# Performance work log

Measured on AMD Instinct MI355X. Metric: run time of the kernel, lower is better.

The kernel has to match this reference:

```python
import jax, jax.numpy as jnp
import numpy as np

B, C, H, W = 4, 256, 48, 48
NH = 4                 # num_heads
HD = C // NH           # head_dim = 64
KD = HD // 2           # key_dim = 32 (attn_ratio=0.5)
QKV_C = C + 2 * KD * NH  # 512
FF = 2 * C             # 512
EPS = 1e-3             # ultralytics BatchNorm2d eps


def _bn(x, g, b, m, v):
    # eval-mode BatchNorm2d over channel dim 1 of NCHW
    s = g / jnp.sqrt(v + EPS)
    return x * s[:, None, None] + (b - m * s)[:, None, None]


def _conv1x1(x, w):
    # w: [out_c, in_c]
    return jnp.einsum('bchw,oc->bohw', x, w)


def _dwconv3x3(x, w):
    # depthwise 3x3, padding 1; w: [C, 1, 3, 3]
    return jax.lax.conv_general_dilated(
        x, w, (1, 1), [(1, 1), (1, 1)],
        dimension_numbers=('NCHW', 'OIHW', 'NCHW'),
        feature_group_count=C)


def setup_inputs() -> dict:
    key = jax.random.key(0)
    ks = jax.random.split(key, 32)
    d = {}
    d['x'] = jax.random.normal(ks[0], (B, C, H, W), dtype=jnp.float32)

    def bn_params(i, ch):
        g = 0.5 + jax.random.uniform(ks[i], (ch,), dtype=jnp.float32)
        b = 0.1 * jax.random.normal(ks[i + 1], (ch,), dtype=jnp.float32)
        m = 0.1 * jax.random.normal(ks[i + 2], (ch,), dtype=jnp.float32)
        v = 0.5 + jax.random.uniform(ks[i + 3], (ch,), dtype=jnp.float32)
        return g, b, m, v

    d['qkv_w'] = 0.05 * jax.random.normal(ks[1], (QKV_C, C), dtype=jnp.float32)
    d['qkv_g'], d['qkv_b'], d['qkv_m'], d['qkv_v'] = bn_params(2, QKV_C)
    d['pe_w'] = 0.1 * jax.random.normal(ks[6], (C, 1, 3, 3), dtype=jnp.float32)
    d['pe_g'], d['pe_b'], d['pe_m'], d['pe_v'] = bn_params(7, C)
    d['proj_w'] = 0.05 * jax.random.normal(ks[11], (C, C), dtype=jnp.float32)
    d['proj_g'], d['proj_b'], d['proj_m'], d['proj_v'] = bn_params(12, C)
    d['f1_w'] = 0.05 * jax.random.normal(ks[16], (FF, C), dtype=jnp.float32)
    d['f1_g'], d['f1_b'], d['f1_m'], d['f1_v'] = bn_params(17, FF)
    d['f2_w'] = 0.05 * jax.random.normal(ks[21], (C, FF), dtype=jnp.float32)
    d['f2_g'], d['f2_b'], d['f2_m'], d['f2_v'] = bn_params(22, C)
    return d


def reference(x, qkv_w, qkv_g, qkv_b, qkv_m, qkv_v,
              pe_w, pe_g, pe_b, pe_m, pe_v,
              proj_w, proj_g, proj_b, proj_m, proj_v,
              f1_w, f1_g, f1_b, f1_m, f1_v,
              f2_w, f2_g, f2_b, f2_m, f2_v):
    b, c, h, w = x.shape
    n = h * w
    # --- Attention ---
    qkv = _bn(_conv1x1(x, qkv_w), qkv_g, qkv_b, qkv_m, qkv_v)
    qkv = qkv.reshape(b, NH, 2 * KD + HD, n)
    q = qkv[:, :, :KD]            # [b, nh, kd, n]
    k = qkv[:, :, KD:2 * KD]      # [b, nh, kd, n]
    v = qkv[:, :, 2 * KD:]        # [b, nh, hd, n]
    attn = jnp.einsum('bhkn,bhkm->bhnm', q, k) * (KD ** -0.5)
    attn = jax.nn.softmax(attn, axis=-1)
    o = jnp.einsum('bhdm,bhnm->bhdn', v, attn).reshape(b, c, h, w)
    pe = _bn(_dwconv3x3(v.reshape(b, c, h, w), pe_w), pe_g, pe_b, pe_m, pe_v)
    attn_out = _bn(_conv1x1(o + pe, proj_w), proj_g, proj_b, proj_m, proj_v)
    x = x + attn_out  # shortcut
    # --- FFN ---
    f = _conv1x1(x, f1_w)
    f = _bn(f, f1_g, f1_b, f1_m, f1_v)
    f = f * jax.nn.sigmoid(f)  # SiLU
    f = _bn(_conv1x1(f, f2_w), f2_g, f2_b, f2_m, f2_v)
    return x + f  # shortcut
```

## Files before the change

kernel.cpp:

```cpp
#include <hip/hip_runtime.h>
#include <math.h>

#define Bb   4
#define Cc   256
#define Hh   48
#define Ww   48
#define NNp  2304
#define Rr   9216
#define NHd  4
#define QKVC 512
#define EPSf 1e-3f

typedef unsigned int   u32;
typedef unsigned short u16;
typedef __attribute__((ext_vector_type(8))) __bf16 bf16x8;
typedef __attribute__((ext_vector_type(4))) float  f32x4;

#if __has_builtin(__builtin_amdgcn_exp2f)
#define EXP2F(x) __builtin_amdgcn_exp2f(x)
#else
#define EXP2F(x) __expf((x) * 0.6931471805599453f)
#endif

__device__ __forceinline__ u16 f2bf(float f) {
    u32 u = __float_as_uint(f);
    u = (u + 0x7fffu + ((u >> 16) & 1u)) >> 16;
    return (u16)u;
}
__device__ __forceinline__ float bf2f(u16 h) {
    return __uint_as_float((u32)h << 16);
}
__device__ __forceinline__ u32 pk2bf(float a, float b) {
    union { __bf16 h; u16 u; } ua, ub;
    ua.h = (__bf16)a; ub.h = (__bf16)b;
    return (u32)ua.u | ((u32)ub.u << 16);
}
__device__ __forceinline__ void gload16(const void* gsrc, void* ldst) {
    __builtin_amdgcn_global_load_lds(
        (const __attribute__((address_space(1))) u32*)gsrc,
        (__attribute__((address_space(3))) u32*)ldst, 16, 0, 0);
}

__global__ __launch_bounds__(64)
void prep_all(const float* __restrict__ W0, const float* __restrict__ g0, const float* __restrict__ b0, const float* __restrict__ m0, const float* __restrict__ v0, u16* __restrict__ Wb0, float* __restrict__ bi0,
              const float* __restrict__ W1, const float* __restrict__ g1, const float* __restrict__ b1, const float* __restrict__ m1, const float* __restrict__ v1, u16* __restrict__ Wb1, float* __restrict__ bi1,
              const float* __restrict__ W2, const float* __restrict__ g2, const float* __restrict__ b2, const float* __restrict__ m2, const float* __restrict__ v2, u16* __restrict__ Wb2, float* __restrict__ bi2,
              const float* __restrict__ W3, const float* __restrict__ g3, const float* __restrict__ b3, const float* __restrict__ m3, const float* __restrict__ v3, u16* __restrict__ Wb3, float* __restrict__ bi3)
{
    const int bid = blockIdx.x;
    const float *W, *gp, *bp, *mp, *vp;
    u16* Wb; float* bias;
    int K = 256, oc;
    float c = 1.f;
    if (bid < 512) {
        oc = bid; W = W0; gp = g0; bp = b0; mp = m0; vp = v0; Wb = Wb0; bias = bi0;
        if ((oc & 127) < 32) c = 0.17677669529663687f * 1.4426950408889634f;
    } else if (bid < 768) {
        oc = bid - 512; W = W1; gp = g1; bp = b1; mp = m1; vp = v1; Wb = Wb1; bias = bi1;
    } else if (bid < 1280) {
        oc = bid - 768; W = W2; gp = g2; bp = b2; mp = m2; vp = v2; Wb = Wb2; bias = bi2;
    } else {
        oc = bid - 1280; W = W3; gp = g3; bp = b3; mp = m3; vp = v3; Wb = Wb3; bias = bi3;
        K = 512;
    }
    const int lane = threadIdx.x;
    const float s = gp[oc] * rsqrtf(vp[oc] + EPSf);
    if (lane == 0) bias[oc] = (bp[oc] - mp[oc] * s) * c;
    const float sc = s * c;
    for (int k0 = lane * 4; k0 < K; k0 += 256) {
        const float4 w = *(const float4*)(W + (size_t)oc * K + k0);
        u32 lo = (u32)f2bf(w.x * sc) | ((u32)f2bf(w.y * sc) << 16);
        u32 hi = (u32)f2bf(w.z * sc) | ((u32)f2bf(w.w * sc) << 16);
        *(uint2*)(Wb + (size_t)oc * K + k0) = make_uint2(lo, hi);
    }
}

__global__ __launch_bounds__(256)
void cvt_x(const float* __restrict__ x, u16* __restrict__ Xt)
{
    const int b = blockIdx.z, c0 = blockIdx.y * 64, n0 = blockIdx.x * 64;
    __shared__ float tile[64][65];
    const int tid = threadIdx.x;
    {
        const int n = tid & 63, cl = tid >> 6;
        #pragma unroll
        for (int cc = 0; cc < 16; ++cc) {
            const int c = cc * 4 + cl;
            tile[c][n] = x[((size_t)b * Cc + c0 + c) * NNp + n0 + n];
        }
    }
    __syncthreads();
    {
        const int n = tid >> 2, q = tid & 3;
        #pragma unroll
        for (int j = 0; j < 2; ++j) {
            const int ch = q * 2 + j, c = ch * 8;
            u32 w[4];
            #pragma unroll
            for (int e = 0; e < 4; ++e)
                w[e] = (u32)f2bf(tile[c + 2*e][n]) | ((u32)f2bf(tile[c + 2*e + 1][n]) << 16);
            *(uint4*)(Xt + ((size_t)b * NNp + n0 + n) * Cc + c0 + c)
                = make_uint4(w[0], w[1], w[2], w[3]);
        }
    }
}

template<int BN_, int FN_, int MODE>
__global__ __launch_bounds__(256)
void gemm_mfma(const u16* __restrict__ A, const u16* __restrict__ Bx,
               const float* __restrict__ bias, const float* __restrict__ resid,
               float* __restrict__ Yf, u16* __restrict__ Yt, int M, int K)
{
    constexpr int WN = FN_ * 16;
    const int r0 = blockIdx.x * BN_;
    const int m0 = blockIdx.y * 128;
    const int tid = threadIdx.x;
    const int lane = tid & 63, wid = tid >> 6;
    const int g = lane >> 4, i16 = lane & 15;
    const int wr = wid >> 1, wc = wid & 1;

    __shared__ __align__(16) u16 Al[2][4][128][8];
    __shared__ __align__(16) u16 Bl[2][4][BN_][8];

    f32x4 acc[4][FN_];
    #pragma unroll
    for (int i = 0; i < 4; ++i)
        #pragma unroll
        for (int j = 0; j < FN_; ++j) acc[i][j] = (f32x4){0.f, 0.f, 0.f, 0.f};

    #pragma unroll
    for (int ii = 0; ii < 2; ++ii) {
        const int ci = ii * 256 + tid;
        gload16(A + (size_t)(m0 + (ci & 127)) * K + (ci >> 7) * 8,
                (u16*)&Al[0][0][0][0] + (size_t)ci * 8);
    }
    if (BN_ == 128) {
        #pragma unroll
        for (int ii = 0; ii < 2; ++ii) {
            const int ci = ii * 256 + tid;
            gload16(Bx + (size_t)(r0 + (ci & 127)) * K + (ci >> 7) * 8,
                    (u16*)&Bl[0][0][0][0] + (size_t)ci * 8);
        }
    } else {
        gload16(Bx + (size_t)(r0 + (tid & 63)) * K + (tid >> 6) * 8,
                (u16*)&Bl[0][0][0][0] + (size_t)tid * 8);
    }
    __syncthreads();

    int buf = 0;
    for (int k0 = 0; k0 < K; k0 += 32) {
        if (k0 + 32 < K) {
            const int kn = k0 + 32;
            #pragma unroll
            for (int ii = 0; ii < 2; ++ii) {
                const int ci = ii * 256 + tid;
                gload16(A + (size_t)(m0 + (ci & 127)) * K + kn + (ci >> 7) * 8,
                        (u16*)&Al[buf ^ 1][0][0][0] + (size_t)ci * 8);
            }
            if (BN_ == 128) {
                #pragma unroll
                for (int ii = 0; ii < 2; ++ii) {
                    const int ci = ii * 256 + tid;
                    gload16(Bx + (size_t)(r0 + (ci & 127)) * K + kn + (ci >> 7) * 8,
                            (u16*)&Bl[buf ^ 1][0][0][0] + (size_t)ci * 8);
                }
            } else {
                gload16(Bx + (size_t)(r0 + (tid & 63)) * K + kn + (tid >> 6) * 8,
                        (u16*)&Bl[buf ^ 1][0][0][0] + (size_t)tid * 8);
            }
        }
        bf16x8 af[4], bf[FN_];
        #pragma unroll
        for (int ao = 0; ao < 4; ++ao)
            af[ao] = *(const bf16x8*)&Al[buf][g][wr * 64 + ao * 16 + i16][0];
        #pragma unroll
        for (int bo = 0; bo < FN_; ++bo)
            bf[bo] = *(const bf16x8*)&Bl[buf][g][wc * WN + bo * 16 + i16][0];
        __builtin_amdgcn_s_setprio(1);
        #pragma unroll
        for (int ao = 0; ao < 4; ++ao)
            #pragma unroll
            for (int bo = 0; bo < FN_; ++bo)
                acc[ao][bo] = __builtin_amdgcn_mfma_f32_16x16x32_bf16(
                    af[ao], bf[bo], acc[ao][bo], 0, 0, 0);
        __builtin_amdgcn_s_setprio(0);
        __syncthreads();
        buf ^= 1;
    }

    const int b  = r0 / NNp;
    const int nb = r0 - b * NNp;
    #pragma unroll
    for (int ao = 0; ao < 4; ++ao) {
        const int oc0 = m0 + wr * 64 + ao * 16 + g * 4;
        const float4 t4 = *(const float4*)(bias + oc0);
        #pragma unroll
        for (int bo = 0; bo < FN_; ++bo) {
            const int nloc = wc * WN + bo * 16 + i16;
            float y[4];
            y[0] = acc[ao][bo][0] + t4.x;  y[1] = acc[ao][bo][1] + t4.y;
            y[2] = acc[ao][bo][2] + t4.z;  y[3] = acc[ao][bo][3] + t4.w;
            if (MODE == 1 || MODE == 3) {
                const int n = nb + nloc;
                const size_t base = ((size_t)b * M + oc0) * NNp + n;
                #pragma unroll
                for (int r = 0; r < 4; ++r) {
                    y[r] += resid[base + (size_t)r * NNp];
                    Yf[base + (size_t)r * NNp] = y[r];
                }
            }
            if (MODE == 2) {
                #pragma unroll
                for (int r = 0; r < 4; ++r) y[r] = y[r] / (1.f + __expf(-y[r]));
            }
            if (MODE != 3) {
                const size_t rG = (size_t)(r0 + nloc);
                u32 lo = (u32)f2bf(y[0]) | ((u32)f2bf(y[1]) << 16);
                u32 hi = (u32)f2bf(y[2]) | ((u32)f2bf(y[3]) << 16);
                *(uint2*)(Yt + rG * M + oc0) = make_uint2(lo, hi);
            }
        }
    }
}

__global__ __launch_bounds__(256)
void repack_v(const u16* __restrict__ Yt, u16* __restrict__ Vb)
{
    const int m0 = blockIdx.x * 64;
    const int h = blockIdx.y, b = blockIdx.z;
    const int bh = b * NHd + h;
    __shared__ u16 vt[64][72];
    const int tid = threadIdx.x;
    #pragma unroll
    for (int ii = 0; ii < 2; ++ii) {
        const int mm = ii * 32 + (tid >> 3);
        const int ch = tid & 7;
        *(uint4*)&vt[mm][ch * 8] =
            *(const uint4*)(Yt + ((size_t)b * NNp + m0 + mm) * QKVC + h * 128 + 64 + ch * 8);
    }
    __syncthreads();
    const int d = tid >> 2, mq = tid & 3;
    #pragma unroll
    for (int j = 0; j < 2; ++j) {
        const int mc = mq * 2 + j;
        u32 w[4];
        #pragma unroll
        for (int e = 0; e < 4; ++e)
            w[e] = (u32)vt[mc * 8 + 2*e][d] | ((u32)vt[mc * 8 + 2*e + 1][d] << 16);
        *(uint4*)(Vb + ((size_t)bh * 64 + d) * NNp + m0 + mc * 8)
            = make_uint4(w[0], w[1], w[2], w[3]);
    }
}

__global__ __launch_bounds__(256)
void attn_mfma(const u16* __restrict__ Yt, const u16* __restrict__ Vb,
               u16* __restrict__ Ot)
{
    __shared__ __align__(16) u16 Klds[2][4][128][8];
    __shared__ __align__(16) u16 Vlds[2][64][16][8];
    __shared__ __align__(16) u32 Plds[4][2][16][36];

    const int tid  = threadIdx.x;
    const int wid  = tid >> 6;
    const int lane = tid & 63;
    const int g    = lane >> 4;
    const int i16  = lane & 15;
    const int ksl  = wid >> 1;
    const int qh   = wid & 1;

    const int h = blockIdx.y, b = blockIdx.z;
    const int bh = b * NHd + h;
    const size_t bG = (size_t)b * NNp;
    const u16* Vg = Vb + (size_t)bh * 64 * NNp;

    const int nq0 = blockIdx.x * 64 + qh * 32 + i16;
    bf16x8 qfrag[2];
    qfrag[0] = *(const bf16x8*)(Yt + (bG + nq0) * QKVC + h * 128 + g * 8);
    qfrag[1] = *(const bf16x8*)(Yt + (bG + nq0 + 16) * QKVC + h * 128 + g * 8);

    bf16x8 ones;
    { uint4 ov = make_uint4(0x3f803f80u, 0x3f803f80u, 0x3f803f80u, 0x3f803f80u);
      ones = *(bf16x8*)&ov; }

    const f32x4 zero = {0.f, 0.f, 0.f, 0.f};
    f32x4 oacc[2][4];
    f32x4 lacc[2];
    #pragma unroll
    for (int f = 0; f < 2; ++f) {
        lacc[f] = zero;
        #pragma unroll
        for (int d = 0; d < 4; ++d) oacc[f][d] = zero;
    }
    float m_run[2] = {-1e30f, -1e30f};

    #pragma unroll
    for (int ii = 0; ii < 2; ++ii) {
        const int ci = ii * 256 + tid;
        gload16(Yt + (bG + (ci & 127)) * QKVC + h * 128 + 32 + (ci >> 7) * 8,
                (u16*)&Klds[0][0][0][0] + (size_t)ci * 8);
    }
    #pragma unroll
    for (int ii = 0; ii < 4; ++ii) {
        const int idx = ii * 256 + tid;
        const int d = idx >> 4, cp = idx & 15;
        gload16(Vg + (size_t)d * NNp + (cp ^ (d & 7)) * 8,
                (u16*)&Vlds[0][0][0][0] + (size_t)idx * 8);
    }
    __syncthreads();

    int cur = 0;
    for (int t = 0; t < 18; ++t) {
        if (t < 17) {
            const int m0 = (t + 1) * 128;
            #pragma unroll
            for (int ii = 0; ii < 2; ++ii) {
                const int ci = ii * 256 + tid;
                gload16(Yt + (bG + m0 + (ci & 127)) * QKVC + h * 128 + 32 + (ci >> 7) * 8,
                        (u16*)&Klds[cur ^ 1][0][0][0] + (size_t)ci * 8);
            }
            #pragma unroll
            for (int ii = 0; ii < 4; ++ii) {
                const int idx = ii * 256 + tid;
                const int d = idx >> 4, cp = idx & 15;
                gload16(Vg + (size_t)d * NNp + m0 + (cp ^ (d & 7)) * 8,
                        (u16*)&Vlds[cur ^ 1][0][0][0] + (size_t)idx * 8);
            }
        }

        bf16x8 kf[4];
        #pragma unroll
        for (int j = 0; j < 4; ++j)
            kf[j] = *(const bf16x8*)&Klds[cur][g][ksl * 64 + 16 * j + i16][0];

        f32x4 sac[2][4];
        __builtin_amdgcn_s_setprio(1);
        #pragma unroll
        for (int f = 0; f < 2; ++f)
            #pragma unroll
            for (int j = 0; j < 4; ++j)
                sac[f][j] = __builtin_amdgcn_mfma_f32_16x16x32_bf16(
                    kf[j], qfrag[f], zero, 0, 0, 0);
        __builtin_amdgcn_s_setprio(0);

        #pragma unroll
        for (int f = 0; f < 2; ++f) {
            float pm = sac[f][0][0];
            #pragma unroll
            for (int j = 0; j < 4; ++j)
                #pragma unroll
                for (int r = 0; r < 4; ++r) pm = fmaxf(pm, sac[f][j][r]);
            pm = fmaxf(pm, __shfl_xor(pm, 16));
            pm = fmaxf(pm, __shfl_xor(pm, 32));

            if (!__all(pm <= m_run[f] + 8.f)) {
                const float mn = fmaxf(m_run[f], pm);
                const float fc = EXP2F(m_run[f] - mn);
                m_run[f] = mn;
                lacc[f][0] *= fc; lacc[f][1] *= fc;
                lacc[f][2] *= fc; lacc[f][3] *= fc;
                #pragma unroll
                for (int d = 0; d < 4; ++d) {
                    oacc[f][d][0] *= fc; oacc[f][d][1] *= fc;
                    oacc[f][d][2] *= fc; oacc[f][d][3] *= fc;
                }
            }

            u32* prow = &Plds[wid][f][i16][0];
            #pragma unroll
            for (int j = 0; j < 4; ++j) {
                const float p0 = EXP2F(sac[f][j][0] - m_run[f]);
                const float p1 = EXP2F(sac[f][j][1] - m_run[f]);
                const float p2 = EXP2F(sac[f][j][2] - m_run[f]);
                const float p3 = EXP2F(sac[f][j][3] - m_run[f]);
                *(uint2*)&prow[8 * j + 2 * g] = make_uint2(pk2bf(p0, p1), pk2bf(p2, p3));
            }
        }

        __builtin_amdgcn_s_setprio(1);
        #pragma unroll
        for (int s = 0; s < 2; ++s) {
            const bf16x8 pf0 = *(const bf16x8*)&Plds[wid][0][i16][16 * s + 4 * g];
            const bf16x8 pf1 = *(const bf16x8*)&Plds[wid][1][i16][16 * s + 4 * g];
            lacc[0] = __builtin_amdgcn_mfma_f32_16x16x32_bf16(ones, pf0, lacc[0], 0, 0, 0);
            lacc[1] = __builtin_amdgcn_mfma_f32_16x16x32_bf16(ones, pf1, lacc[1], 0, 0, 0);
            const int cv = ksl * 8 + 4 * s + g;
            #pragma unroll
            for (int db = 0; db < 4; ++db) {
                const bf16x8 vf = *(const bf16x8*)&Vlds[cur][db * 16 + i16][cv ^ (i16 & 7)][0];
                oacc[0][db] = __builtin_amdgcn_mfma_f32_16x16x32_bf16(vf, pf0, oacc[0][db], 0, 0, 0);
                oacc[1][db] = __builtin_amdgcn_mfma_f32_16x16x32_bf16(vf, pf1, oacc[1][db], 0, 0, 0);
            }
        }
        __builtin_amdgcn_s_setprio(0);

        __syncthreads();
        cur ^= 1;
    }

    float* Ml = (float*)&Vlds[0][0][0][0];
    if (wid >= 2) {
        #pragma unroll
        for (int f = 0; f < 2; ++f) {
            float* dst = Ml + ((size_t)((qh * 2 + f) * 64 + lane)) * 20;
            dst[0] = m_run[f];
            dst[1] = lacc[f][0];
            #pragma unroll
            for (int db = 0; db < 4; ++db)
                #pragma unroll
                for (int e = 0; e < 4; ++e)
                    dst[2 + db * 4 + e] = oacc[f][db][e];
        }
    }
    __syncthreads();
    if (wid < 2) {
        #pragma unroll
        for (int f = 0; f < 2; ++f) {
            const float* src = Ml + ((size_t)((qh * 2 + f) * 64 + lane)) * 20;
            const float m2 = src[0], l2 = src[1];
            const float mn = fmaxf(m_run[f], m2);
            const float fa = EXP2F(m_run[f] - mn);
            const float fb = EXP2F(m2 - mn);
            const float linv = 1.f / (lacc[f][0] * fa + l2 * fb);
            u16* ob = Ot + (bG + nq0 + f * 16) * Cc + h * 64;
            #pragma unroll
            for (int db = 0; db < 4; ++db) {
                const float y0 = (oacc[f][db][0] * fa + src[2 + db * 4 + 0] * fb) * linv;
                const float y1 = (oacc[f][db][1] * fa + src[2 + db * 4 + 1] * fb) * linv;
                const float y2 = (oacc[f][db][2] * fa + src[2 + db * 4 + 2] * fb) * linv;
                const float y3 = (oacc[f][db][3] * fa + src[2 + db * 4 + 3] * fb) * linv;
                *(uint2*)(ob + db * 16 + g * 4) =
                    make_uint2(pk2bf(y0, y1), pk2bf(y2, y3));
            }
        }
    }
}

__global__ __launch_bounds__(256)
void pe_bn(const u16* __restrict__ Yt, const float* __restrict__ pw,
           const float* __restrict__ gg, const float* __restrict__ bb,
           const float* __restrict__ mm, const float* __restrict__ vv,
           u16* __restrict__ Ot)
{
    const int tid = threadIdx.x;
    const int h = blockIdx.y, b = blockIdx.z;
    const int p = blockIdx.x * 32 + (tid >> 3);
    const int ch = tid & 7;
    const int c0 = h * 64 + ch * 8;
    const int yy = p / Ww, xx = p - yy * Ww;

    float acc[8];
    #pragma unroll
    for (int j = 0; j < 8; ++j) acc[j] = 0.f;

    #pragma unroll
    for (int dy = -1; dy <= 1; ++dy) {
        const int Y = yy + dy;
        if (Y < 0 || Y >= Hh) continue;
        #pragma unroll
        for (int dx = -1; dx <= 1; ++dx) {
            const int X = xx + dx;
            if (X < 0 || X >= Ww) continue;
            const uint4 raw = *(const uint4*)(Yt +
                ((size_t)b * NNp + Y * Ww + X) * QKVC + h * 128 + 64 + ch * 8);
            const u32* rw = (const u32*)&raw;
            #pragma unroll
            for (int j = 0; j < 8; ++j) {
                const u16 hv = (u16)(rw[j >> 1] >> (16 * (j & 1)));
                acc[j] += pw[(size_t)(c0 + j) * 9 + (dy + 1) * 3 + (dx + 1)] * bf2f(hv);
            }
        }
    }

    u16* dst = Ot + ((size_t)b * NNp + p) * Cc + c0;
    uint4 old = *(uint4*)dst;
    u32* ow = (u32*)&old;
    u32 res[4];
    #pragma unroll
    for (int e = 0; e < 4; ++e) {
        u16 r0, r1;
        {
            const int j = 2 * e;
            const float s = gg[c0 + j] * rsqrtf(vv[c0 + j] + EPSf);
            const float t = bb[c0 + j] - mm[c0 + j] * s;
            r0 = f2bf(bf2f((u16)(ow[e] & 0xffff)) + acc[j] * s + t);
        }
        {
            const int j = 2 * e + 1;
            const float s = gg[c0 + j] * rsqrtf(vv[c0 + j] + EPSf);
            const float t = bb[c0 + j] - mm[c0 + j] * s;
            r1 = f2bf(bf2f((u16)(ow[e] >> 16)) + acc[j] * s + t);
        }
        res[e] = (u32)r0 | ((u32)r1 << 16);
    }
    *(uint4*)dst = make_uint4(res[0], res[1], res[2], res[3]);
}

extern "C" void kernel_launch(void* const* d_in, const int* in_sizes, int n_in,
                              void* d_out, int out_size, void* d_ws, size_t ws_size,
                              hipStream_t stream)
{
    const float* x      = (const float*)d_in[0];
    const float* qkv_w  = (const float*)d_in[1];
    const float* qkv_g  = (const float*)d_in[2];
    const float* qkv_b  = (const float*)d_in[3];
    const float* qkv_m  = (const float*)d_in[4];
    const float* qkv_v  = (const float*)d_in[5];
    const float* pe_w   = (const float*)d_in[6];
    const float* pe_g   = (const float*)d_in[7];
    const float* pe_b   = (const float*)d_in[8];
    const float* pe_m   = (const float*)d_in[9];
    const float* pe_v   = (const float*)d_in[10];
    const float* proj_w = (const float*)d_in[11];
    const float* proj_g = (const float*)d_in[12];
    const float* proj_b = (const float*)d_in[13];
    const float* proj_m = (const float*)d_in[14];
    const float* proj_v = (const float*)d_in[15];
    const float* f1_w   = (const float*)d_in[16];
    const float* f1_g   = (const float*)d_in[17];
    const float* f1_b   = (const float*)d_in[18];
    const float* f1_m   = (const float*)d_in[19];
    const float* f1_v   = (const float*)d_in[20];
    const float* f2_w   = (const float*)d_in[21];
    const float* f2_g   = (const float*)d_in[22];
    const float* f2_b   = (const float*)d_in[23];
    const float* f2_m   = (const float*)d_in[24];
    const float* f2_v   = (const float*)d_in[25];

    char* wsb = (char*)d_ws;
    u16*   Yt   = (u16*)(wsb);
    u16*   Xt   = (u16*)(wsb + 9437184);
    u16*   Vb   = (u16*)(wsb + 14155776);
    u16*   Ot   = (u16*)(wsb + 18874368);
    float* x1f  = (float*)(wsb + 23592960);
    u16*   Wq   = (u16*)(wsb + 33030144);
    u16*   Wp   = (u16*)(wsb + 33292288);
    u16*   W1   = (u16*)(wsb + 33423360);
    u16*   W2   = (u16*)(wsb + 33685504);
    float* biq  = (float*)(wsb + 33947648);
    float* bip  = (float*)(wsb + 33949696);
    float* bi1  = (float*)(wsb + 33950720);
    float* bi2  = (float*)(wsb + 33952768);
    u16*   Ft   = Yt;
    u16*   X1t  = Xt;
    float* out  = (float*)d_out;

    prep_all<<<dim3(1536), dim3(64), 0, stream>>>(
        qkv_w, qkv_g, qkv_b, qkv_m, qkv_v, Wq, biq,
        proj_w, proj_g, proj_b, proj_m, proj_v, Wp, bip,
        f1_w, f1_g, f1_b, f1_m, f1_v, W1, bi1,
        f2_w, f2_g, f2_b, f2_m, f2_v, W2, bi2);
    cvt_x<<<dim3(36, 4, 4), dim3(256), 0, stream>>>(x, Xt);

    gemm_mfma<128, 4, 0><<<dim3(72, 4), dim3(256), 0, stream>>>(
        Wq, Xt, biq, nullptr, nullptr, Yt, QKVC, 256);

    repack_v<<<dim3(36, 4, 4), dim3(256), 0, stream>>>(Yt, Vb);
    attn_mfma<<<dim3(36, 4, 4), dim3(256), 0, stream>>>(Yt, Vb, Ot);
    pe_bn<<<dim3(72, 4, 4), dim3(256), 0, stream>>>(Yt, pe_w, pe_g, pe_b, pe_m, pe_v, Ot);

    gemm_mfma<64, 2, 1><<<dim3(144, 2), dim3(256), 0, stream>>>(
        Wp, Ot, bip, x, x1f, X1t, Cc, 256);

    gemm_mfma<128, 4, 2><<<dim3(72, 4), dim3(256), 0, stream>>>(
        W1, X1t, bi1, nullptr, nullptr, Ft, QKVC, 256);

    gemm_mfma<64, 2, 3><<<dim3(144, 2), dim3(256), 0, stream>>>(
        W2, Ft, bi2, x1f, out, nullptr, Cc, 512);
}
```

Measured before the change: 166.9 us.

## Restructure attention into 128-thread blocks with no key split and swizzled grid

The attention kernel moves from 256-thread blocks, where four waves split 64 queries and two key halves and then merge partial softmax state through LDS, to 128-thread blocks where each wave owns 16 queries and walks all keys in 64-key tiles. This removes the cross-wave merge, halves register accumulators per wave, and launches 1152 blocks on a 1D grid with an XCD-aware swizzle so blocks sharing a (batch, head) tend to land on the same die. In exchange K/V tiles are loaded twice as often per query, the loop runs 36 iterations with a barrier each, and global K/V traffic per query roughly doubles.

```diff
diff --git a/kernel.cpp b/kernel.cpp
--- a/kernel.cpp
+++ b/kernel.cpp
@@ -252,143 +252,128 @@
     }
 }
 
-__global__ __launch_bounds__(256)
+__global__ __launch_bounds__(128)
 void attn_mfma(const u16* __restrict__ Yt, const u16* __restrict__ Vb,
                u16* __restrict__ Ot)
 {
-    __shared__ __align__(16) u16 Klds[2][4][128][8];
-    __shared__ __align__(16) u16 Vlds[2][64][16][8];
-    __shared__ __align__(16) u32 Plds[4][2][16][36];
+    __shared__ __align__(16) u16 Klds[2][4][64][8];
+    __shared__ __align__(16) u16 Vlds[2][64][8][8];
+    __shared__ __align__(16) u32 Plds[2][16][36];
 
     const int tid  = threadIdx.x;
     const int wid  = tid >> 6;
     const int lane = tid & 63;
     const int g    = lane >> 4;
     const int i16  = lane & 15;
-    const int ksl  = wid >> 1;
-    const int qh   = wid & 1;
-
-    const int h = blockIdx.y, b = blockIdx.z;
-    const int bh = b * NHd + h;
+
+    const int wg  = blockIdx.x;
+    const int swz = (wg & 7) * 144 + (wg >> 3);
+    const int xq  = swz % 72;
+    const int bh  = swz / 72;
+    const int h   = bh & 3, b = bh >> 2;
+
     const size_t bG = (size_t)b * NNp;
     const u16* Vg = Vb + (size_t)bh * 64 * NNp;
 
-    const int nq0 = blockIdx.x * 64 + qh * 32 + i16;
-    bf16x8 qfrag[2];
-    qfrag[0] = *(const bf16x8*)(Yt + (bG + nq0) * QKVC + h * 128 + g * 8);
-    qfrag[1] = *(const bf16x8*)(Yt + (bG + nq0 + 16) * QKVC + h * 128 + g * 8);
+    const int nq = xq * 32 + wid * 16 + i16;
+    const bf16x8 qfrag = *(const bf16x8*)(Yt + (bG + nq) * QKVC + h * 128 + g * 8);
 
     bf16x8 ones;
     { uint4 ov = make_uint4(0x3f803f80u, 0x3f803f80u, 0x3f803f80u, 0x3f803f80u);
       ones = *(bf16x8*)&ov; }
 
     const f32x4 zero = {0.f, 0.f, 0.f, 0.f};
-    f32x4 oacc[2][4];
-    f32x4 lacc[2];
-    #pragma unroll
-    for (int f = 0; f < 2; ++f) {
-        lacc[f] = zero;
-        #pragma unroll
-        for (int d = 0; d < 4; ++d) oacc[f][d] = zero;
-    }
-    float m_run[2] = {-1e30f, -1e30f};
+    f32x4 oacc[4];
+    f32x4 lacc = zero;
+    #pragma unroll
+    for (int d = 0; d < 4; ++d) oacc[d] = zero;
+    float m_run = -1e30f;
 
     #pragma unroll
     for (int ii = 0; ii < 2; ++ii) {
-        const int ci = ii * 256 + tid;
-        gload16(Yt + (bG + (ci & 127)) * QKVC + h * 128 + 32 + (ci >> 7) * 8,
+        const int ci = ii * 128 + tid;
+        gload16(Yt + (bG + (ci & 63)) * QKVC + h * 128 + 32 + (ci >> 6) * 8,
                 (u16*)&Klds[0][0][0][0] + (size_t)ci * 8);
     }
     #pragma unroll
     for (int ii = 0; ii < 4; ++ii) {
-        const int idx = ii * 256 + tid;
-        const int d = idx >> 4, cp = idx & 15;
+        const int idx = ii * 128 + tid;
+        const int d = idx >> 3, cp = idx & 7;
         gload16(Vg + (size_t)d * NNp + (cp ^ (d & 7)) * 8,
                 (u16*)&Vlds[0][0][0][0] + (size_t)idx * 8);
     }
     __syncthreads();
 
     int cur = 0;
-    for (int t = 0; t < 18; ++t) {
-        if (t < 17) {
-            const int m0 = (t + 1) * 128;
+    for (int t = 0; t < 36; ++t) {
+        if (t < 35) {
+            const int m0 = (t + 1) * 64;
             #pragma unroll
             for (int ii = 0; ii < 2; ++ii) {
-                const int ci = ii * 256 + tid;
-                gload16(Yt + (bG + m0 + (ci & 127)) * QKVC + h * 128 + 32 + (ci >> 7) * 8,
+                const int ci = ii * 128 + tid;
+                gload16(Yt + (bG + m0 + (ci & 63)) * QKVC + h * 128 + 32 + (ci >> 6) * 8,
                         (u16*)&Klds[cur ^ 1][0][0][0] + (size_t)ci * 8);
             }
             #pragma unroll
             for (int ii = 0; ii < 4; ++ii) {
-                const int idx = ii * 256 + tid;
-                const int d = idx >> 4, cp = idx & 15;
+                const int idx = ii * 128 + tid;
+                const int d = idx >> 3, cp = idx & 7;
                 gload16(Vg + (size_t)d * NNp + m0 + (cp ^ (d & 7)) * 8,
                         (u16*)&Vlds[cur ^ 1][0][0][0] + (size_t)idx * 8);
             }
         }
 
-        bf16x8 kf[4];
+        f32x4 sac[4];
+        __builtin_amdgcn_s_setprio(1);
+        #pragma unroll
+        for (int j = 0; j < 4; ++j) {
+            const bf16x8 kf = *(const bf16x8*)&Klds[cur][g][16 * j + i16][0];
+            sac[j] = __builtin_amdgcn_mfma_f32_16x16x32_bf16(kf, qfrag, zero, 0, 0, 0);
+        }
+        __builtin_amdgcn_s_setprio(0);
+
+        float pm = sac[0][0];
         #pragma unroll
         for (int j = 0; j < 4; ++j)
-            kf[j] = *(const bf16x8*)&Klds[cur][g][ksl * 64 + 16 * j + i16][0];
-
-        f32x4 sac[2][4];
+            #pragma unroll
+            for (int r = 0; r < 4; ++r) pm = fmaxf(pm, sac[j][r]);
+        pm = fmaxf(pm, __shfl_xor(pm, 16));
+        pm = fmaxf(pm, __shfl_xor(pm, 32));
+
+        if (!__all(pm <= m_run + 8.f)) {
+            const float mn = fmaxf(m_run, pm);
+            const float fc = EXP2F(m_run - mn);
+            m_run = mn;
+            lacc[0] *= fc; lacc[1] *= fc; lacc[2] *= fc; lacc[3] *= fc;
+            #pragma unroll
+            for (int d = 0; d < 4; ++d) {
+                oacc[d][0] *= fc; oacc[d][1] *= fc;
+                oacc[d][2] *= fc; oacc[d][3] *= fc;
+            }
+        }
+
+        {
+            u32* prow = &Plds[wid][i16][0];
+            #pragma unroll
+            for (int j = 0; j < 4; ++j) {
+                const float p0 = EXP2F(sac[j][0] - m_run);
+                const float p1 = EXP2F(sac[j][1] - m_run);
+                const float p2 = EXP2F(sac[j][2] - m_run);
+                const float p3 = EXP2F(sac[j][3] - m_run);
+                *(uint2*)&prow[8 * j + 2 * g] = make_uint2(pk2bf(p0, p1), pk2bf(p2, p3));
+            }
+        }
+
+        const int d7 = i16 & 7;
         __builtin_amdgcn_s_setprio(1);
         #pragma unroll
-        for (int f = 0; f < 2; ++f)
-            #pragma unroll
-            for (int j = 0; j < 4; ++j)
-                sac[f][j] = __builtin_amdgcn_mfma_f32_16x16x32_bf16(
-                    kf[j], qfrag[f], zero, 0, 0, 0);
-        __builtin_amdgcn_s_setprio(0);
-
-        #pragma unroll
-        for (int f = 0; f < 2; ++f) {
-            float pm = sac[f][0][0];
-            #pragma unroll
-            for (int j = 0; j < 4; ++j)
-                #pragma unroll
-                for (int r = 0; r < 4; ++r) pm = fmaxf(pm, sac[f][j][r]);
-            pm = fmaxf(pm, __shfl_xor(pm, 16));
-            pm = fmaxf(pm, __shfl_xor(pm, 32));
-
-            if (!__all(pm <= m_run[f] + 8.f)) {
-                const float mn = fmaxf(m_run[f], pm);
-                const float fc = EXP2F(m_run[f] - mn);
-                m_run[f] = mn;
-                lacc[f][0] *= fc; lacc[f][1] *= fc;
-                lacc[f][2] *= fc; lacc[f][3] *= fc;
-                #pragma unroll
-                for (int d = 0; d < 4; ++d) {
-                    oacc[f][d][0] *= fc; oacc[f][d][1] *= fc;
-                    oacc[f][d][2] *= fc; oacc[f][d][3] *= fc;
-                }
-            }
-
-            u32* prow = &Plds[wid][f][i16][0];
-            #pragma unroll
-            for (int j = 0; j < 4; ++j) {
-                const float p0 = EXP2F(sac[f][j][0] - m_run[f]);
-                const float p1 = EXP2F(sac[f][j][1] - m_run[f]);
-                const float p2 = EXP2F(sac[f][j][2] - m_run[f]);
-                const float p3 = EXP2F(sac[f][j][3] - m_run[f]);
-                *(uint2*)&prow[8 * j + 2 * g] = make_uint2(pk2bf(p0, p1), pk2bf(p2, p3));
-            }
-        }
-
-        __builtin_amdgcn_s_setprio(1);
-        #pragma unroll
         for (int s = 0; s < 2; ++s) {
-            const bf16x8 pf0 = *(const bf16x8*)&Plds[wid][0][i16][16 * s + 4 * g];
-            const bf16x8 pf1 = *(const bf16x8*)&Plds[wid][1][i16][16 * s + 4 * g];
-            lacc[0] = __builtin_amdgcn_mfma_f32_16x16x32_bf16(ones, pf0, lacc[0], 0, 0, 0);
-            lacc[1] = __builtin_amdgcn_mfma_f32_16x16x32_bf16(ones, pf1, lacc[1], 0, 0, 0);
-            const int cv = ksl * 8 + 4 * s + g;
+            const bf16x8 pf = *(const bf16x8*)&Plds[wid][i16][16 * s + 4 * g];
+            lacc = __builtin_amdgcn_mfma_f32_16x16x32_bf16(ones, pf, lacc, 0, 0, 0);
             #pragma unroll
             for (int db = 0; db < 4; ++db) {
-                const bf16x8 vf = *(const bf16x8*)&Vlds[cur][db * 16 + i16][cv ^ (i16 & 7)][0];
-                oacc[0][db] = __builtin_amdgcn_mfma_f32_16x16x32_bf16(vf, pf0, oacc[0][db], 0, 0, 0);
-                oacc[1][db] = __builtin_amdgcn_mfma_f32_16x16x32_bf16(vf, pf1, oacc[1][db], 0, 0, 0);
+                const bf16x8 vf = *(const bf16x8*)&Vlds[cur][db * 16 + i16][(4 * s + g) ^ d7][0];
+                oacc[db] = __builtin_amdgcn_mfma_f32_16x16x32_bf16(vf, pf, oacc[db], 0, 0, 0);
             }
         }
         __builtin_amdgcn_s_setprio(0);
@@ -397,41 +382,13 @@
         cur ^= 1;
     }
 
-    float* Ml = (float*)&Vlds[0][0][0][0];
-    if (wid >= 2) {
-        #pragma unroll
-        for (int f = 0; f < 2; ++f) {
-            float* dst = Ml + ((size_t)((qh * 2 + f) * 64 + lane)) * 20;
-            dst[0] = m_run[f];
-            dst[1] = lacc[f][0];
-            #pragma unroll
-            for (int db = 0; db < 4; ++db)
-                #pragma unroll
-                for (int e = 0; e < 4; ++e)
-                    dst[2 + db * 4 + e] = oacc[f][db][e];
-        }
-    }
-    __syncthreads();
-    if (wid < 2) {
-        #pragma unroll
-        for (int f = 0; f < 2; ++f) {
-            const float* src = Ml + ((size_t)((qh * 2 + f) * 64 + lane)) * 20;
-            const float m2 = src[0], l2 = src[1];
-            const float mn = fmaxf(m_run[f], m2);
-            const float fa = EXP2F(m_run[f] - mn);
-            const float fb = EXP2F(m2 - mn);
-            const float linv = 1.f / (lacc[f][0] * fa + l2 * fb);
-            u16* ob = Ot + (bG + nq0 + f * 16) * Cc + h * 64;
-            #pragma unroll
-            for (int db = 0; db < 4; ++db) {
-                const float y0 = (oacc[f][db][0] * fa + src[2 + db * 4 + 0] * fb) * linv;
-                const float y1 = (oacc[f][db][1] * fa + src[2 + db * 4 + 1] * fb) * linv;
-                const float y2 = (oacc[f][db][2] * fa + src[2 + db * 4 + 2] * fb) * linv;
-                const float y3 = (oacc[f][db][3] * fa + src[2 + db * 4 + 3] * fb) * linv;
-                *(uint2*)(ob + db * 16 + g * 4) =
-                    make_uint2(pk2bf(y0, y1), pk2bf(y2, y3));
-            }
-        }
+    const float linv = 1.f / lacc[0];
+    u16* ob = Ot + (bG + nq) * Cc + h * 64;
+    #pragma unroll
+    for (int db = 0; db < 4; ++db) {
+        u32 lo = pk2bf(oacc[db][0] * linv, oacc[db][1] * linv);
+        u32 hi = pk2bf(oacc[db][2] * linv, oacc[db][3] * linv);
+        *(uint2*)(ob + db * 16 + g * 4) = make_uint2(lo, hi);
     }
 }
 
@@ -555,7 +512,7 @@
         Wq, Xt, biq, nullptr, nullptr, Yt, QKVC, 256);
 
     repack_v<<<dim3(36, 4, 4), dim3(256), 0, stream>>>(Yt, Vb);
-    attn_mfma<<<dim3(36, 4, 4), dim3(256), 0, stream>>>(Yt, Vb, Ot);
+    attn_mfma<<<dim3(1152), dim3(128), 0, stream>>>(Yt, Vb, Ot);
     pe_bn<<<dim3(72, 4, 4), dim3(256), 0, stream>>>(Yt, pe_w, pe_g, pe_b, pe_m, pe_v, Ot);
 
     gemm_mfma<64, 2, 1><<<dim3(144, 2), dim3(256), 0, stream>>>(
```

Measured after the change: 151.7 us. 1.1x faster.
